# Performance work log

Hardware: AMD Instinct MI355X
Metric: run time of the kernel (lower is better)

## Reference

```python
import jax, jax.numpy as jnp
import numpy as np

H_IMG, W_IMG = 128, 128            # image size (init arg)
FX, FY = 120.0, 120.0              # camera intrinsics (read from COLMAP cfg in original __init__)
CX, CY = 64.0, 64.0
N_GAUSS = 65536
N_POSES = 2
EPS = 1e-8


def quat2mat(q):
    q = q / jnp.linalg.norm(q)
    w, x, y, z = q[0], q[1], q[2], q[3]
    return jnp.stack([
        jnp.stack([1 - 2 * (y * y + z * z), 2 * (x * y - z * w), 2 * (x * z + y * w)]),
        jnp.stack([2 * (x * y + z * w), 1 - 2 * (x * x + z * z), 2 * (y * z - x * w)]),
        jnp.stack([2 * (x * z - y * w), 2 * (y * z + x * w), 1 - 2 * (x * x + y * y)]),
    ])


def _forward(positions, colors, opacities, scales, qvec, tvec, tile_hw, chunk_gauss):
    HW = H_IMG * W_IMG
    step = tile_hw * tile_hw          # pixels per tile (contiguous in flat row-major order)
    n_tiles = HW // step
    N = positions.shape[0]
    n_chunks = N // chunk_gauss
    xs = jnp.arange(W_IMG, dtype=jnp.float32)
    ys = jnp.arange(H_IMG, dtype=jnp.float32)
    yy, xx = jnp.meshgrid(ys, xs, indexing='ij')
    px = xx.reshape(-1)               # [HW] pixel x coords
    py = yy.reshape(-1)               # [HW] pixel y coords
    var_c = (scales[:, 0] ** 2).reshape(n_chunks, chunk_gauss)
    op_c = opacities[:, 0].reshape(n_chunks, chunk_gauss)
    col_c = colors.reshape(n_chunks, chunk_gauss, 3)

    def render_pose(q, t):
        R = quat2mat(q)
        cam = positions @ R.T + t                                 # [N,3] camera-space points
        uv = jnp.stack([cam[:, 0] / cam[:, 2] * FX + CX,
                        cam[:, 1] / cam[:, 2] * FY + CY], 1)      # [N,2] pixel-space centers
        uv_c = uv.reshape(n_chunks, chunk_gauss, 2)

        def body(acc, chunk):
            uvg, vg, og, cg = chunk                               # [C,2],[C],[C],[C,3]
            d2 = (px[None, :] - uvg[:, 0:1]) ** 2 + (py[None, :] - uvg[:, 1:2]) ** 2  # [C,HW]
            w = og[:, None] * jnp.exp(-0.5 * d2 / vg[:, None])    # [C,HW] splat weights
            return (acc[0] + w.T @ cg, acc[1] + w.sum(0)), None

        init = (jnp.zeros((HW, 3), jnp.float32), jnp.zeros((HW,), jnp.float32))
        (num, den), _ = jax.lax.scan(body, init, (uv_c, var_c, op_c, col_c))
        # original adds 1e-8 to the denominator once per gaussian chunk
        img = num / (den + n_chunks * EPS)[:, None]               # [HW,3] normalized blend
        # per tile of `step` flat pixels: [step,3].T -> [3,tile_hw,tile_hw]
        return img.reshape(n_tiles, step, 3).transpose(0, 2, 1).reshape(n_tiles, 3, tile_hw, tile_hw)

    out = jax.vmap(render_pose)(qvec, tvec)                       # [B, n_tiles, 3, th, th]
    return out.reshape(-1, 3, tile_hw, tile_hw)


def setup_inputs() -> dict:
    key = jax.random.key(0)
    ks = jax.random.split(key, 6)
    positions = jax.random.normal(ks[0], (N_GAUSS, 3), jnp.float32) * 1.5
    positions = positions.at[:, 2].set(jnp.abs(positions[:, 2]) + 4.0)  # keep z>0 (in front of camera)
    colors = jax.random.uniform(ks[1], (N_GAUSS, 3), jnp.float32)
    opacities = jax.random.uniform(ks[2], (N_GAUSS, 1), jnp.float32)
    scales = jax.random.uniform(ks[3], (N_GAUSS, 1), jnp.float32) * 2.0 + 1.0  # var strictly > 0
    qvec = jax.random.normal(ks[4], (N_POSES, 4), jnp.float32)
    tvec = jax.random.normal(ks[5], (N_POSES, 3), jnp.float32) * 0.1
    return {"positions": positions, "colors": colors, "opacities": opacities,
            "scales": scales, "qvec": qvec, "tvec": tvec,
            "tile_hw": 32, "chunk_gauss": 4096}


def reference(positions, colors, opacities, scales, qvec, tvec, tile_hw, chunk_gauss):
    return _forward(positions, colors, opacities, scales, qvec, tvec, tile_hw, chunk_gauss)
```

## Files before the change

kernel.cpp:

```cpp
#include <hip/hip_runtime.h>


#define H_IMG 128
#define W_IMG 128
#define FX_C 120.0f
#define FY_C 120.0f
#define CX_C 64.0f
#define CY_C 64.0f
#define NG 65536
#define SLAB 512
#define KSPLIT 128
#define NCHUNK 8
#define APAD 72
#define NEG_HALF_LOG2E -0.72134752044448170f
#define EPS_TOT 1.6e-7f

#if __has_builtin(__builtin_amdgcn_exp2f)
#define EXP2(x) __builtin_amdgcn_exp2f(x)
#else
#define EXP2(x) exp2f(x)
#endif

typedef __attribute__((ext_vector_type(8))) short short8;
typedef __attribute__((ext_vector_type(4))) float f32x4;

__device__ __forceinline__ unsigned bfpk2(float a, float b) {
    return __builtin_amdgcn_perm(__float_as_uint(b) + 0x8000u,
                                 __float_as_uint(a) + 0x8000u,
                                 0x07060302u);
}
__device__ __forceinline__ ushort bf16u(float v) {
    return (ushort)((__float_as_uint(v) + 0x8000u) >> 16);
}

__global__ void zero_accum_kernel(float* __restrict__ p) {
    p[blockIdx.x * 256 + threadIdx.x] = 0.0f;
}

template <bool STORE>
__global__ __launch_bounds__(1024, 4) void render_kernel(
    const float* __restrict__ gpos, const float* __restrict__ gcol,
    const float* __restrict__ gopa, const float* __restrict__ gscl,
    const float* __restrict__ qvec, const float* __restrict__ tvec,
    float* __restrict__ accum,
    ushort* __restrict__ pbuf)
{
    __shared__ ushort A_lds[H_IMG][APAD];
    __shared__ ushort B_lds[512][APAD];
    __shared__ float u_s[SLAB], v_s[SLAB], ke_s[SLAB];
    __shared__ float wc_s[4][SLAB];

    const int split = blockIdx.x;
    const int pose  = blockIdx.y;
    const int tid   = threadIdx.x;

    float q0 = qvec[pose*4+0], q1 = qvec[pose*4+1], q2 = qvec[pose*4+2], q3 = qvec[pose*4+3];
    float rn = rsqrtf(q0*q0 + q1*q1 + q2*q2 + q3*q3);
    float qw = q0*rn, qx = q1*rn, qy = q2*rn, qz = q3*rn;
    float r00 = 1.0f-2.0f*(qy*qy+qz*qz), r01 = 2.0f*(qx*qy-qz*qw), r02 = 2.0f*(qx*qz+qy*qw);
    float r10 = 2.0f*(qx*qy+qz*qw), r11 = 1.0f-2.0f*(qx*qx+qz*qz), r12 = 2.0f*(qy*qz-qx*qw);
    float r20 = 2.0f*(qx*qz-qy*qw), r21 = 2.0f*(qy*qz+qx*qw), r22 = 1.0f-2.0f*(qx*qx+qy*qy);
    float tx = tvec[pose*3+0], ty = tvec[pose*3+1], tz = tvec[pose*3+2];

    if (tid < SLAB) {
        int g = split*SLAB + tid;
        float p0 = gpos[g*3+0], p1 = gpos[g*3+1], p2 = gpos[g*3+2];
        float cxm = r00*p0 + r01*p1 + r02*p2 + tx;
        float cym = r10*p0 + r11*p1 + r12*p2 + ty;
        float czm = r20*p0 + r21*p1 + r22*p2 + tz;
        float iz  = 1.0f / czm;
        u_s[tid] = cxm*iz*FX_C + CX_C;
        v_s[tid] = cym*iz*FY_C + CY_C;
        float s  = gscl[g];
        ke_s[tid] = NEG_HALF_LOG2E / (s*s);
        float og = gopa[g];
        wc_s[0][tid] = og * gcol[g*3+0];
        wc_s[1][tid] = og * gcol[g*3+1];
        wc_s[2][tid] = og * gcol[g*3+2];
        wc_s[3][tid] = og;
    }
    __syncthreads();

    const int lane = tid & 63;
    const int wave = tid >> 6;
    const int wm   = wave >> 3;
    const int wn8  = wave & 7;

    const bool isB = (tid < 512);
    const int st   = tid & 511;
    const int g4   = (st & 15) << 2;
    const int grp  = st >> 4;

    const int frow = lane & 15;
    const int kqd  = (lane >> 4) << 3;

    f32x4 acc[4][4] = {};

    for (int ch = 0; ch < NCHUNK; ++ch) {
        const int gb = (ch << 6) + g4;
        const float4 kv = *(const float4*)&ke_s[gb];
        if (isB) {
            const float4 uv = *(const float4*)&u_s[gb];
            float e[4][4];
            #pragma unroll
            for (int xi = 0; xi < 4; ++xi) {
                const float xf = (float)(grp*4 + xi);
                float d;
                d = xf - uv.x; e[xi][0] = EXP2(kv.x*d*d);
                d = xf - uv.y; e[xi][1] = EXP2(kv.y*d*d);
                d = xf - uv.z; e[xi][2] = EXP2(kv.z*d*d);
                d = xf - uv.w; e[xi][3] = EXP2(kv.w*d*d);
            }
            #pragma unroll
            for (int c = 0; c < 4; ++c) {
                const float4 wv = *(const float4*)&wc_s[c][gb];
                #pragma unroll
                for (int xi = 0; xi < 4; ++xi) {
                    uint2 pk;
                    pk.x = bfpk2(e[xi][0]*wv.x, e[xi][1]*wv.y);
                    pk.y = bfpk2(e[xi][2]*wv.z, e[xi][3]*wv.w);
                    *(uint2*)&B_lds[(c << 7) + grp*4 + xi][g4] = pk;
                }
            }
        } else {
            const float4 vv = *(const float4*)&v_s[gb];
            #pragma unroll
            for (int yi = 0; yi < 4; ++yi) {
                const float yf = (float)(grp*4 + yi);
                float d, f0, f1, f2, f3;
                d = yf - vv.x; f0 = EXP2(kv.x*d*d);
                d = yf - vv.y; f1 = EXP2(kv.y*d*d);
                d = yf - vv.z; f2 = EXP2(kv.z*d*d);
                d = yf - vv.w; f3 = EXP2(kv.w*d*d);
                uint2 pk;
                pk.x = bfpk2(f0, f1); pk.y = bfpk2(f2, f3);
                *(uint2*)&A_lds[grp*4 + yi][g4] = pk;
            }
        }
        __syncthreads();
        #pragma unroll
        for (int ks = 0; ks < 2; ++ks) {
            const int kcol = ks*32 + kqd;
            short8 a[4], b[4];
            #pragma unroll
            for (int mt = 0; mt < 4; ++mt)
                a[mt] = *(const short8*)&A_lds[wm*64 + mt*16 + frow][kcol];
            #pragma unroll
            for (int nt = 0; nt < 4; ++nt)
                b[nt] = *(const short8*)&B_lds[wn8*64 + nt*16 + frow][kcol];
            #pragma unroll
            for (int mt = 0; mt < 4; ++mt)
                #pragma unroll
                for (int nt = 0; nt < 4; ++nt)
                    acc[mt][nt] = __builtin_amdgcn_mfma_f32_16x16x32_bf16(a[mt], b[nt], acc[mt][nt], 0, 0, 0);
        }
        __syncthreads();
    }

    const int q4 = (lane >> 4) << 2;
    const int n0 = wn8*64 + (lane & 15);
    if (STORE) {
        ushort* bp = pbuf + ((size_t)(pose*KSPLIT + split) * H_IMG + wm*64) * 512 + n0;
        #pragma unroll
        for (int mt = 0; mt < 4; ++mt)
            #pragma unroll
            for (int nt = 0; nt < 4; ++nt)
                #pragma unroll
                for (int r = 0; r < 4; ++r)
                    bp[(size_t)(mt*16 + q4 + r)*512 + nt*16] = bf16u(acc[mt][nt][r]);
    } else {
        float* bp = accum + ((size_t)(pose*H_IMG + wm*64) * 512) + n0;
        #pragma unroll
        for (int mt = 0; mt < 4; ++mt)
            #pragma unroll
            for (int nt = 0; nt < 4; ++nt)
                #pragma unroll
                for (int r = 0; r < 4; ++r)
                    atomicAdd(bp + (size_t)(mt*16 + q4 + r)*512 + nt*16, acc[mt][nt][r]);
    }
}

__global__ __launch_bounds__(1024) void reduce_norm_kernel(
    const ushort* __restrict__ pbuf, float* __restrict__ out)
{
    __shared__ float red[2][512];
    const int b  = blockIdx.x;
    const int p  = b >> 7;
    const int y  = b & 127;
    const int t  = threadIdx.x;
    const int sg = t >> 9;
    const int n  = t & 511;

    const ushort* base = pbuf + ((size_t)(p*KSPLIT + sg*64) * H_IMG + y) * 512 + n;
    float s = 0.0f;
    #pragma unroll 8
    for (int i = 0; i < 64; ++i) {
        unsigned us = base[(size_t)i * (H_IMG*512)];
        s += __uint_as_float(us << 16);
    }
    red[sg][n] = s;
    __syncthreads();

    if (t < 384) {
        const int c = t >> 7, x = t & 127;
        float den = red[0][384 + x] + red[1][384 + x];
        float num = red[0][t]       + red[1][t];
        float inv = 1.0f / (den + EPS_TOT);
        int tt = y >> 3;
        int q  = ((y & 7) << 7) + x;
        out[(size_t)((p*16 + tt)*3 + c) * 1024 + q] = num * inv;
    }
}

__global__ void normalize_kernel(const float* __restrict__ acc, float* __restrict__ out) {
    int idx = blockIdx.x * 256 + threadIdx.x;
    int x = idx & 127;
    int y = (idx >> 7) & 127;
    int p = idx >> 14;
    const float* base = acc + (size_t)(p*128 + y) * 512;
    float inv = 1.0f / (base[384 + x] + EPS_TOT);
    int t = y >> 3;
    int q = ((y & 7) << 7) + x;
    float* ob = out + (size_t)((p*16 + t)*3) * 1024 + q;
    ob[0]    = base[x]       * inv;
    ob[1024] = base[128 + x] * inv;
    ob[2048] = base[256 + x] * inv;
}

extern "C" void kernel_launch(void* const* d_in, const int* in_sizes, int n_in,
                              void* d_out, int out_size, void* d_ws, size_t ws_size,
                              hipStream_t stream) {
    const float* gpos = (const float*)d_in[0];
    const float* gcol = (const float*)d_in[1];
    const float* gopa = (const float*)d_in[2];
    const float* gscl = (const float*)d_in[3];
    const float* qv   = (const float*)d_in[4];
    const float* tv   = (const float*)d_in[5];
    float* out = (float*)d_out;

    const size_t need = (size_t)2 * KSPLIT * H_IMG * 512 * sizeof(ushort);

    if (ws_size >= need) {
        ushort* pbuf = (ushort*)d_ws;
        render_kernel<true><<<dim3(KSPLIT, 2), dim3(1024), 0, stream>>>(
            gpos, gcol, gopa, gscl, qv, tv, nullptr, pbuf);
        reduce_norm_kernel<<<dim3(256), dim3(1024), 0, stream>>>(pbuf, out);
    } else {
        float* acc = (float*)d_ws;
        zero_accum_kernel<<<dim3(512), dim3(256), 0, stream>>>(acc);
        render_kernel<false><<<dim3(KSPLIT, 2), dim3(1024), 0, stream>>>(
            gpos, gcol, gopa, gscl, qv, tv, acc, nullptr);
        normalize_kernel<<<dim3(128), dim3(256), 0, stream>>>(acc, out);
    }
}
```

Measured before the change: 108.4 us.

## Double-buffer splat staging with MFMA and vectorize the split-K reduction

The render kernel now stages half-width chunks of 32 gaussians into two LDS buffers. Chunk N+1's exp2 weights are built while MFMA consumes chunk N, so one barrier per chunk replaces two. Separately, the reduce kernel reads 16-byte vectors of packed bf16 partials and combines them through a 16-way shared-memory tree instead of scalar 2-byte loads. The cost is more chunk iterations with smaller K per step and some extra LDS traffic in the reduction.

```diff
diff --git a/kernel.cpp b/kernel.cpp
--- a/kernel.cpp
+++ b/kernel.cpp
@@ -10,8 +10,9 @@
 #define NG 65536
 #define SLAB 512
 #define KSPLIT 128
-#define NCHUNK 8
-#define APAD 72
+#define KC 32
+#define NCH 16
+#define KPAD 40
 #define NEG_HALF_LOG2E -0.72134752044448170f
 #define EPS_TOT 1.6e-7f
 
@@ -45,8 +46,8 @@
     float* __restrict__ accum,
     ushort* __restrict__ pbuf)
 {
-    __shared__ ushort A_lds[H_IMG][APAD];
-    __shared__ ushort B_lds[512][APAD];
+    __shared__ ushort A_lds[2][H_IMG][KPAD];
+    __shared__ ushort B_lds[2][512][KPAD];
     __shared__ float u_s[SLAB], v_s[SLAB], ke_s[SLAB];
     __shared__ float wc_s[4][SLAB];
 
@@ -88,74 +89,83 @@
 
     const bool isB = (tid < 512);
     const int st   = tid & 511;
-    const int g4   = (st & 15) << 2;
-    const int grp  = st >> 4;
+    const int g4   = (st & 7) << 2;
+    const int rg   = st >> 3;
 
     const int frow = lane & 15;
-    const int kqd  = (lane >> 4) << 3;
+    const int kq   = (lane >> 4) << 3;
 
     f32x4 acc[4][4] = {};
 
-    for (int ch = 0; ch < NCHUNK; ++ch) {
-        const int gb = (ch << 6) + g4;
-        const float4 kv = *(const float4*)&ke_s[gb];
-        if (isB) {
-            const float4 uv = *(const float4*)&u_s[gb];
-            float e[4][4];
-            #pragma unroll
-            for (int xi = 0; xi < 4; ++xi) {
-                const float xf = (float)(grp*4 + xi);
-                float d;
-                d = xf - uv.x; e[xi][0] = EXP2(kv.x*d*d);
-                d = xf - uv.y; e[xi][1] = EXP2(kv.y*d*d);
-                d = xf - uv.z; e[xi][2] = EXP2(kv.z*d*d);
-                d = xf - uv.w; e[xi][3] = EXP2(kv.w*d*d);
-            }
-            #pragma unroll
-            for (int c = 0; c < 4; ++c) {
-                const float4 wv = *(const float4*)&wc_s[c][gb];
-                #pragma unroll
-                for (int xi = 0; xi < 4; ++xi) {
-                    uint2 pk;
-                    pk.x = bfpk2(e[xi][0]*wv.x, e[xi][1]*wv.y);
-                    pk.y = bfpk2(e[xi][2]*wv.z, e[xi][3]*wv.w);
-                    *(uint2*)&B_lds[(c << 7) + grp*4 + xi][g4] = pk;
-                }
-            }
-        } else {
-            const float4 vv = *(const float4*)&v_s[gb];
-            #pragma unroll
-            for (int yi = 0; yi < 4; ++yi) {
-                const float yf = (float)(grp*4 + yi);
-                float d, f0, f1, f2, f3;
-                d = yf - vv.x; f0 = EXP2(kv.x*d*d);
-                d = yf - vv.y; f1 = EXP2(kv.y*d*d);
-                d = yf - vv.z; f2 = EXP2(kv.z*d*d);
-                d = yf - vv.w; f3 = EXP2(kv.w*d*d);
-                uint2 pk;
-                pk.x = bfpk2(f0, f1); pk.y = bfpk2(f2, f3);
-                *(uint2*)&A_lds[grp*4 + yi][g4] = pk;
-            }
+#define STAGE_CHUNK(ch, b)                                                     \
+    {                                                                          \
+        const int gb = ((ch) << 5) + g4;                                       \
+        const float4 kv = *(const float4*)&ke_s[gb];                           \
+        if (isB) {                                                             \
+            const float4 uv = *(const float4*)&u_s[gb];                        \
+            float e[2][4];                                                     \
+            _Pragma("unroll")                                                  \
+            for (int xi = 0; xi < 2; ++xi) {                                   \
+                const float xf = (float)(rg*2 + xi);                           \
+                float d;                                                       \
+                d = xf - uv.x; e[xi][0] = EXP2(kv.x*d*d);                      \
+                d = xf - uv.y; e[xi][1] = EXP2(kv.y*d*d);                      \
+                d = xf - uv.z; e[xi][2] = EXP2(kv.z*d*d);                      \
+                d = xf - uv.w; e[xi][3] = EXP2(kv.w*d*d);                      \
+            }                                                                  \
+            _Pragma("unroll")                                                  \
+            for (int c = 0; c < 4; ++c) {                                      \
+                const float4 wv = *(const float4*)&wc_s[c][gb];                \
+                _Pragma("unroll")                                              \
+                for (int xi = 0; xi < 2; ++xi) {                               \
+                    uint2 pk;                                                  \
+                    pk.x = bfpk2(e[xi][0]*wv.x, e[xi][1]*wv.y);                \
+                    pk.y = bfpk2(e[xi][2]*wv.z, e[xi][3]*wv.w);                \
+                    *(uint2*)&B_lds[b][(c << 7) + rg*2 + xi][g4] = pk;         \
+                }                                                              \
+            }                                                                  \
+        } else {                                                               \
+            const float4 vv = *(const float4*)&v_s[gb];                        \
+            _Pragma("unroll")                                                  \
+            for (int yi = 0; yi < 2; ++yi) {                                   \
+                const float yf = (float)(rg*2 + yi);                           \
+                float d, f0, f1, f2, f3;                                       \
+                d = yf - vv.x; f0 = EXP2(kv.x*d*d);                            \
+                d = yf - vv.y; f1 = EXP2(kv.y*d*d);                            \
+                d = yf - vv.z; f2 = EXP2(kv.z*d*d);                            \
+                d = yf - vv.w; f3 = EXP2(kv.w*d*d);                            \
+                uint2 pk;                                                      \
+                pk.x = bfpk2(f0, f1); pk.y = bfpk2(f2, f3);                    \
+                *(uint2*)&A_lds[b][rg*2 + yi][g4] = pk;                        \
+            }                                                                  \
+        }                                                                      \
+    }
+
+    STAGE_CHUNK(0, 0)
+
+    for (int ch = 0; ch < NCH; ++ch) {
+        __syncthreads();
+        if (ch + 1 < NCH) {
+            const int nb = (ch + 1) & 1;
+            STAGE_CHUNK(ch + 1, nb)
         }
-        __syncthreads();
-        #pragma unroll
-        for (int ks = 0; ks < 2; ++ks) {
-            const int kcol = ks*32 + kqd;
+        {
+            const int cb = ch & 1;
             short8 a[4], b[4];
             #pragma unroll
             for (int mt = 0; mt < 4; ++mt)
-                a[mt] = *(const short8*)&A_lds[wm*64 + mt*16 + frow][kcol];
+                a[mt] = *(const short8*)&A_lds[cb][wm*64 + mt*16 + frow][kq];
             #pragma unroll
             for (int nt = 0; nt < 4; ++nt)
-                b[nt] = *(const short8*)&B_lds[wn8*64 + nt*16 + frow][kcol];
+                b[nt] = *(const short8*)&B_lds[cb][wn8*64 + nt*16 + frow][kq];
             #pragma unroll
             for (int mt = 0; mt < 4; ++mt)
                 #pragma unroll
                 for (int nt = 0; nt < 4; ++nt)
                     acc[mt][nt] = __builtin_amdgcn_mfma_f32_16x16x32_bf16(a[mt], b[nt], acc[mt][nt], 0, 0, 0);
         }
-        __syncthreads();
-    }
+    }
+#undef STAGE_CHUNK
 
     const int q4 = (lane >> 4) << 2;
     const int n0 = wn8*64 + (lane & 15);
@@ -183,32 +193,48 @@
 __global__ __launch_bounds__(1024) void reduce_norm_kernel(
     const ushort* __restrict__ pbuf, float* __restrict__ out)
 {
-    __shared__ float red[2][512];
+    __shared__ float red[16][512];
+    __shared__ float tot[512];
     const int b  = blockIdx.x;
     const int p  = b >> 7;
     const int y  = b & 127;
     const int t  = threadIdx.x;
-    const int sg = t >> 9;
-    const int n  = t & 511;
-
-    const ushort* base = pbuf + ((size_t)(p*KSPLIT + sg*64) * H_IMG + y) * 512 + n;
-    float s = 0.0f;
-    #pragma unroll 8
-    for (int i = 0; i < 64; ++i) {
-        unsigned us = base[(size_t)i * (H_IMG*512)];
-        s += __uint_as_float(us << 16);
-    }
-    red[sg][n] = s;
+    const int sg = t >> 6;
+    const int ng = t & 63;
+
+    const uint4* base = (const uint4*)(pbuf +
+        ((size_t)(p*KSPLIT + sg*8) * H_IMG + y) * 512 + ng*8);
+    float s[8] = {};
+    #pragma unroll
+    for (int i = 0; i < 8; ++i) {
+        uint4 v = base[(size_t)i * (H_IMG*512/8)];
+        s[0] += __uint_as_float(v.x << 16);
+        s[1] += __uint_as_float(v.x & 0xFFFF0000u);
+        s[2] += __uint_as_float(v.y << 16);
+        s[3] += __uint_as_float(v.y & 0xFFFF0000u);
+        s[4] += __uint_as_float(v.z << 16);
+        s[5] += __uint_as_float(v.z & 0xFFFF0000u);
+        s[6] += __uint_as_float(v.w << 16);
+        s[7] += __uint_as_float(v.w & 0xFFFF0000u);
+    }
+    #pragma unroll
+    for (int j = 0; j < 8; ++j) red[sg][ng*8 + j] = s[j];
+    __syncthreads();
+
+    if (t < 512) {
+        float acc = 0.0f;
+        #pragma unroll
+        for (int g = 0; g < 16; ++g) acc += red[g][t];
+        tot[t] = acc;
+    }
     __syncthreads();
 
     if (t < 384) {
         const int c = t >> 7, x = t & 127;
-        float den = red[0][384 + x] + red[1][384 + x];
-        float num = red[0][t]       + red[1][t];
-        float inv = 1.0f / (den + EPS_TOT);
+        float inv = 1.0f / (tot[384 + x] + EPS_TOT);
         int tt = y >> 3;
         int q  = ((y & 7) << 7) + x;
-        out[(size_t)((p*16 + tt)*3 + c) * 1024 + q] = num * inv;
+        out[(size_t)((p*16 + tt)*3 + c) * 1024 + q] = tot[t] * inv;
     }
 }
 
```

New measurement: 107.5 us, median of 2. Within noise of the previous version (-0.8%).
